# Performance work log

Hardware: AMD Instinct MI355X
Metric: run time of the kernel (lower is better)

The kernel has to match this reference:

```python
import jax, jax.numpy as jnp
import numpy as np

N, E, G = 50000, 500000, 64
IN, HID, HEADS, DH, OUT = 128, 128, 8, 16, 256


def setup_inputs() -> dict:
    key = jax.random.key(0)
    ks = jax.random.split(key, 20)
    w = lambda k, s, sc=0.05: jax.random.normal(k, s, dtype=jnp.float32) * sc
    return {
        'feature': jax.random.normal(ks[0], (N, IN), dtype=jnp.float32),
        'W_gc1': w(ks[1], (IN, HID)), 'b_gc1': jnp.zeros((HID,), jnp.float32),
        'W_gc2': w(ks[2], (HID, HID)), 'b_gc2': jnp.zeros((HID,), jnp.float32),
        'W_src': w(ks[3], (3, HID, HID)), 'b_src': jnp.zeros((3, HID), jnp.float32),
        'W_dst': w(ks[4], (3, HID, HID)), 'b_dst': jnp.zeros((3, HID), jnp.float32),
        'attn': w(ks[5], (3, HEADS, DH), 0.1),
        'Wc1': w(ks[6], (HID, HID)), 'bc1': jnp.zeros((HID,), jnp.float32),
        'Wc2': w(ks[7], (HID, HID // 2)), 'bc2': jnp.zeros((HID // 2,), jnp.float32),
        'Wc3': w(ks[8], (HID // 2, OUT)), 'bc3': jnp.zeros((OUT,), jnp.float32),
        'src': jax.random.randint(ks[9], (E,), 0, N, dtype=jnp.int32),
        'dst': jax.random.randint(ks[10], (E,), 0, N, dtype=jnp.int32),
        'node2graph': jnp.sort(jax.random.randint(ks[11], (N,), 0, G, dtype=jnp.int32)),
    }


def reference(feature, W_gc1, b_gc1, W_gc2, b_gc2, W_src, b_src, W_dst, b_dst, attn,
              Wc1, bc1, Wc2, bc2, Wc3, bc3, src, dst, node2graph):
    ones = jnp.ones((E,), jnp.float32)
    # DGL GraphConv norm='both': src normalized by out-degree, dst by in-degree
    ns = jnp.maximum(jax.ops.segment_sum(ones, src, N), 1.0) ** -0.5
    nd = jnp.maximum(jax.ops.segment_sum(ones, dst, N), 1.0) ** -0.5

    def graph_conv(h, W, b):
        m = (h * ns[:, None]) @ W                 # mult W before aggregation (in>=out)
        agg = jax.ops.segment_sum(m[src], dst, N) # copy_u + sum reduce
        return agg * nd[:, None] + b

    h = jax.nn.relu(graph_conv(feature, W_gc1, b_gc1))
    h = jax.nn.relu(graph_conv(h, W_gc2, b_gc2))

    def gatv2(h, Ws, bs, Wd, bd, a):
        fs = (h @ Ws + bs).reshape(N, HEADS, DH)
        fd = (h @ Wd + bd).reshape(N, HEADS, DH)
        e = jax.nn.leaky_relu(fs[src] + fd[dst], 0.2)   # [E,H,D]
        logit = jnp.einsum('ehd,hd->eh', e, a)          # [E,H]
        m = jax.ops.segment_max(logit, dst, N)          # edge-softmax over dst
        p = jnp.exp(logit - m[dst])
        s = jax.ops.segment_sum(p, dst, N)
        alpha = p / s[dst]                              # [E,H]
        out = jax.ops.segment_sum(alpha[:, :, None] * fs[src], dst, N)
        out = out + h.reshape(N, HEADS, DH)             # identity residual (in==H*D)
        return jax.nn.relu(out).reshape(N, HID)

    for i in range(3):
        h = gatv2(h, W_src[i], b_src[i], W_dst[i], b_dst[i], attn[i])

    hg = jax.ops.segment_max(h, node2graph, G)          # dgl.max_nodes -> [G,HID]
    z = jax.nn.relu(hg @ Wc1 + bc1)
    z = jax.nn.relu(z @ Wc2 + bc2)
    return z @ Wc3 + bc3
```

## Files before the change

kernel.cpp:

```cpp
#include <hip/hip_runtime.h>
#include <hip/hip_bf16.h>

#define NN 50000
#define EE 500000
#define GG 64
#define HIDD 128
#define HEADS 8
#define DHH 16
#define NBLK ((NN + 255) / 256)
#define RTILES 3128
#define GEMM_GRID 391

typedef __bf16 bf16x8 __attribute__((ext_vector_type(8)));
typedef float f32x4 __attribute__((ext_vector_type(4)));

__device__ inline float rowsum8(float y) {
  int t;
  t = __builtin_amdgcn_mov_dpp(__float_as_int(y), 0xB1, 0xF, 0xF, true);  y += __int_as_float(t);
  t = __builtin_amdgcn_mov_dpp(__float_as_int(y), 0x4E, 0xF, 0xF, true);  y += __int_as_float(t);
  t = __builtin_amdgcn_mov_dpp(__float_as_int(y), 0x141, 0xF, 0xF, true); y += __int_as_float(t);
  return y;
}

__device__ inline float2 unpk2(unsigned u) {
  return make_float2(__uint_as_float(u << 16), __uint_as_float(u & 0xFFFF0000u));
}

__device__ inline int frag_off(int row, int kc) {
  return (row >> 4) * 2048 + (kc >> 2) * 512 + ((row & 15) + (kc & 3) * 16) * 8;
}

__global__ void deg_kernel(const int* __restrict__ src, const int* __restrict__ dst,
                           int* __restrict__ outdeg, int* __restrict__ indeg) {
  int i = blockIdx.x * blockDim.x + threadIdx.x;
  int stride = gridDim.x * blockDim.x;
  for (; i < EE; i += stride) {
    atomicAdd(&outdeg[src[i]], 1);
    atomicAdd(&indeg[dst[i]], 1);
  }
}

__global__ void norm_kernel(const int* __restrict__ outdeg, float* __restrict__ ns) {
  int i = blockIdx.x * blockDim.x + threadIdx.x;
  if (i < NN) ns[i] = rsqrtf((float)max(outdeg[i], 1));
}

__global__ __launch_bounds__(256) void scan1_kernel(const int* __restrict__ deg,
                                                    int* __restrict__ excl,
                                                    int* __restrict__ bsum) {
  __shared__ int buf[256];
  int t = threadIdx.x;
  int idx = blockIdx.x * 256 + t;
  int v = (idx < NN) ? deg[idx] : 0;
  buf[t] = v;
  __syncthreads();
#pragma unroll
  for (int off = 1; off < 256; off <<= 1) {
    int tmp = (t >= off) ? buf[t - off] : 0;
    __syncthreads();
    buf[t] += tmp;
    __syncthreads();
  }
  if (idx < NN) excl[idx] = buf[t] - v;
  if (t == 255) bsum[blockIdx.x] = buf[255];
}

__global__ __launch_bounds__(256) void scan2_kernel(int* __restrict__ bsum) {
  __shared__ int buf[256];
  int t = threadIdx.x;
  int v = (t < NBLK) ? bsum[t] : 0;
  buf[t] = v;
  __syncthreads();
#pragma unroll
  for (int off = 1; off < 256; off <<= 1) {
    int tmp = (t >= off) ? buf[t - off] : 0;
    __syncthreads();
    buf[t] += tmp;
    __syncthreads();
  }
  if (t < NBLK) bsum[t] = buf[t] - v;
}

__global__ __launch_bounds__(256) void scan3_kernel(int* __restrict__ excl,
                                                    const int* __restrict__ bsum,
                                                    int* __restrict__ cursor) {
  int idx = blockIdx.x * 256 + threadIdx.x;
  if (idx < NN) {
    int v = excl[idx] + bsum[blockIdx.x];
    excl[idx] = v;
    cursor[idx] = v;
  }
}

__global__ void bin_kernel(const int* __restrict__ src, const int* __restrict__ dst,
                           int* __restrict__ cursor, int* __restrict__ csr_src) {
  int i = blockIdx.x * blockDim.x + threadIdx.x;
  int stride = gridDim.x * blockDim.x;
  for (; i < EE; i += stride) {
    int pos = atomicAdd(&cursor[dst[i]], 1);
    csr_src[pos] = src[i];
  }
}

__global__ __launch_bounds__(256) void split_w_kernel(
    const float* __restrict__ W_gc1, const float* __restrict__ W_gc2,
    const float* __restrict__ W_src, const float* __restrict__ W_dst,
    __bf16* __restrict__ Wblk)
{
  int tid = blockIdx.x * 256 + threadIdx.x;
  int m = tid >> 14;
  int kn = tid & 16383;
  int k = kn >> 7, n = kn & 127;
  const float* Wm = (m == 0) ? W_gc1 : (m == 1) ? W_gc2
                   : (m < 5) ? (W_src + (m - 2) * 16384) : (W_dst + (m - 5) * 16384);
  float v = Wm[kn];
  __bf16 h = (__bf16)v;
  __bf16 l = (__bf16)(v - (float)h);
  int ks = k >> 5;
  int L = n * 32 + ((k >> 3) & 3) * 8 + (k & 7);
  int swz = L ^ ((n & 7) << 3);
  __bf16* dstp = Wblk + m * 32768 + ks * 8192;
  dstp[swz] = h;
  dstp[4096 + swz] = l;
}

__global__ __launch_bounds__(256) void split_h_kernel(
    const float* __restrict__ X, const float* __restrict__ scale,
    __bf16* __restrict__ Ah, __bf16* __restrict__ Al)
{
  int tid = blockIdx.x * 256 + threadIdx.x;
  int row = tid >> 4, kc = tid & 15;
  float v[8];
  if (row < NN) {
    const float4* p = (const float4*)(X + row * 128 + kc * 8);
    float4 a = p[0], b = p[1];
    float s = scale ? scale[row] : 1.f;
    v[0] = a.x * s; v[1] = a.y * s; v[2] = a.z * s; v[3] = a.w * s;
    v[4] = b.x * s; v[5] = b.y * s; v[6] = b.z * s; v[7] = b.w * s;
  } else {
#pragma unroll
    for (int i = 0; i < 8; ++i) v[i] = 0.f;
  }
  bf16x8 hi, lo;
#pragma unroll
  for (int i = 0; i < 8; ++i) {
    __bf16 h = (__bf16)v[i];
    hi[i] = h;
    lo[i] = (__bf16)(v[i] - (float)h);
  }
  int off = frag_off(row, kc);
  *(bf16x8*)(Ah + off) = hi;
  *(bf16x8*)(Al + off) = lo;
}

__global__ __launch_bounds__(256) void gemm_mfma(
    const __bf16* __restrict__ Ah, const __bf16* __restrict__ Al,
    const __bf16* __restrict__ Wmat, const float* __restrict__ bias,
    __bf16* __restrict__ outb)
{
  __shared__ __bf16 wt[8192];
  int tid = threadIdx.x;
  int wid = tid >> 6, lane = tid & 63;
  int wr = wid >> 1, wc = wid & 1;
  int l15 = lane & 15, l4 = lane >> 4;
  f32x4 acc[4][4];
#pragma unroll
  for (int a = 0; a < 4; ++a)
#pragma unroll
    for (int b = 0; b < 4; ++b) acc[a][b] = (f32x4){0.f, 0.f, 0.f, 0.f};
  int rowtile0 = blockIdx.x * 8 + wr * 4;

  for (int ks = 0; ks < 4; ++ks) {
    {
      const bf16x8* g = (const bf16x8*)(Wmat + ks * 8192);
      bf16x8* l = (bf16x8*)wt;
      l[tid]       = g[tid];
      l[tid + 256] = g[tid + 256];
      l[tid + 512] = g[tid + 512];
      l[tid + 768] = g[tid + 768];
    }
    bf16x8 ah[4], al[4];
#pragma unroll
    for (int rt = 0; rt < 4; ++rt) {
      int off = (rowtile0 + rt) * 2048 + ks * 512 + lane * 8;
      ah[rt] = *(const bf16x8*)(Ah + off);
      al[rt] = *(const bf16x8*)(Al + off);
    }
    __syncthreads();
#pragma unroll
    for (int ct = 0; ct < 4; ++ct) {
      int n = wc * 64 + ct * 16 + l15;
      int ei = (n * 32 + l4 * 8) ^ ((n & 7) << 3);
      bf16x8 bh = *(const bf16x8*)(wt + ei);
      bf16x8 bl = *(const bf16x8*)(wt + 4096 + ei);
#pragma unroll
      for (int rt = 0; rt < 4; ++rt) {
        acc[rt][ct] = __builtin_amdgcn_mfma_f32_16x16x32_bf16(ah[rt], bh, acc[rt][ct], 0, 0, 0);
        acc[rt][ct] = __builtin_amdgcn_mfma_f32_16x16x32_bf16(ah[rt], bl, acc[rt][ct], 0, 0, 0);
        acc[rt][ct] = __builtin_amdgcn_mfma_f32_16x16x32_bf16(al[rt], bh, acc[rt][ct], 0, 0, 0);
      }
    }
    __syncthreads();
  }
  int rowbase = blockIdx.x * 128 + wr * 64;
#pragma unroll
  for (int ct = 0; ct < 4; ++ct) {
    int col = wc * 64 + ct * 16 + l15;
    float b = bias ? bias[col] : 0.f;
#pragma unroll
    for (int rt = 0; rt < 4; ++rt) {
#pragma unroll
      for (int r = 0; r < 4; ++r) {
        int row = rowbase + rt * 16 + l4 * 4 + r;
        if (row < NN) outb[row * 128 + col] = (__bf16)(acc[rt][ct][r] + b);
      }
    }
  }
}

__global__ __launch_bounds__(64) void gc_agg_kernel(
    const __bf16* __restrict__ mb, const int* __restrict__ rowoff,
    const int* __restrict__ indeg, const int* __restrict__ csr_src,
    const float2* __restrict__ bias2, const float* __restrict__ nsrow,
    float2* __restrict__ out2,
    __bf16* __restrict__ Ah, __bf16* __restrict__ Al)
{
  __shared__ float buf[128];
  int d = blockIdx.x, c = threadIdx.x;
  int ro = rowoff[d], dg = indeg[d];
  float2 a0 = {0.f, 0.f}, a1 = {0.f, 0.f}, a2 = {0.f, 0.f}, a3 = {0.f, 0.f};
  int j = 0;
  for (; j + 4 <= dg; j += 4) {
    int s0 = csr_src[ro + j], s1 = csr_src[ro + j + 1];
    int s2 = csr_src[ro + j + 2], s3 = csr_src[ro + j + 3];
    float2 v0 = unpk2(*(const unsigned*)(mb + s0 * 128 + 2 * c));
    float2 v1 = unpk2(*(const unsigned*)(mb + s1 * 128 + 2 * c));
    float2 v2 = unpk2(*(const unsigned*)(mb + s2 * 128 + 2 * c));
    float2 v3 = unpk2(*(const unsigned*)(mb + s3 * 128 + 2 * c));
    a0.x += v0.x; a0.y += v0.y; a1.x += v1.x; a1.y += v1.y;
    a2.x += v2.x; a2.y += v2.y; a3.x += v3.x; a3.y += v3.y;
  }
  for (; j < dg; ++j) {
    float2 v = unpk2(*(const unsigned*)(mb + csr_src[ro + j] * 128 + 2 * c));
    a0.x += v.x; a0.y += v.y;
  }
  float accx = (a0.x + a1.x) + (a2.x + a3.x);
  float accy = (a0.y + a1.y) + (a2.y + a3.y);
  float ndv = rsqrtf((float)max(dg, 1));
  float2 b = bias2[c];
  float vx = fmaxf(accx * ndv + b.x, 0.f);
  float vy = fmaxf(accy * ndv + b.y, 0.f);
  if (out2) out2[d * 64 + c] = make_float2(vx, vy);
  if (Ah) {
    float s = nsrow ? nsrow[d] : 1.f;
    ((float2*)buf)[c] = make_float2(vx * s, vy * s);
    __syncthreads();
    if (c < 32) {
      int kc = c & 15;
      int off = frag_off(d, kc);
      bf16x8 pk;
      if (c < 16) {
#pragma unroll
        for (int i = 0; i < 8; ++i) pk[i] = (__bf16)buf[kc * 8 + i];
        *(bf16x8*)(Ah + off) = pk;
      } else {
#pragma unroll
        for (int i = 0; i < 8; ++i) {
          float x = buf[kc * 8 + i];
          __bf16 hh = (__bf16)x;
          pk[i] = (__bf16)(x - (float)hh);
        }
        *(bf16x8*)(Al + off) = pk;
      }
    }
  }
}

__global__ __launch_bounds__(64) void gat_node_kernel(
    const __bf16* __restrict__ fsb,
    const __bf16* __restrict__ fdb,
    const float* __restrict__ attn,
    const int* __restrict__ rowoff, const int* __restrict__ indeg,
    const int* __restrict__ csr_src,
    float2* __restrict__ h2,
    __bf16* __restrict__ Ah, __bf16* __restrict__ Al)
{
  __shared__ float buf[128];
  int d = blockIdx.x, c = threadIdx.x;
  int ro = rowoff[d], dg = indeg[d];
  float2 fdp = unpk2(*(const unsigned*)(fdb + d * 128 + 2 * c));
  float2 ap = ((const float2*)attn)[c];
  float mA = -INFINITY, sA = 0.f; float2 aA = {0.f, 0.f};
  float mB = -INFINITY, sB = 0.f; float2 aB = {0.f, 0.f};
  int j = 0;
  for (; j + 2 <= dg; j += 2) {
    int s0 = csr_src[ro + j], s1 = csr_src[ro + j + 1];
    float2 f0 = unpk2(*(const unsigned*)(fsb + s0 * 128 + 2 * c));
    float2 f1 = unpk2(*(const unsigned*)(fsb + s1 * 128 + 2 * c));
    float x0 = f0.x + fdp.x; x0 = fmaxf(x0, 0.f) + 0.2f * fminf(x0, 0.f);
    float z0 = f0.y + fdp.y; z0 = fmaxf(z0, 0.f) + 0.2f * fminf(z0, 0.f);
    float x1 = f1.x + fdp.x; x1 = fmaxf(x1, 0.f) + 0.2f * fminf(x1, 0.f);
    float z1 = f1.y + fdp.y; z1 = fmaxf(z1, 0.f) + 0.2f * fminf(z1, 0.f);
    float y0 = rowsum8(ap.x * x0 + ap.y * z0);
    float y1 = rowsum8(ap.x * x1 + ap.y * z1);
    float nm = fmaxf(mA, y0);
    float sc = __expf(mA - nm), p = __expf(y0 - nm);
    sA = sA * sc + p; aA.x = aA.x * sc + p * f0.x; aA.y = aA.y * sc + p * f0.y; mA = nm;
    nm = fmaxf(mB, y1);
    sc = __expf(mB - nm); p = __expf(y1 - nm);
    sB = sB * sc + p; aB.x = aB.x * sc + p * f1.x; aB.y = aB.y * sc + p * f1.y; mB = nm;
  }
  if (j < dg) {
    int s0 = csr_src[ro + j];
    float2 f0 = unpk2(*(const unsigned*)(fsb + s0 * 128 + 2 * c));
    float x0 = f0.x + fdp.x; x0 = fmaxf(x0, 0.f) + 0.2f * fminf(x0, 0.f);
    float z0 = f0.y + fdp.y; z0 = fmaxf(z0, 0.f) + 0.2f * fminf(z0, 0.f);
    float y0 = rowsum8(ap.x * x0 + ap.y * z0);
    float nm = fmaxf(mA, y0);
    float sc = __expf(mA - nm), p = __expf(y0 - nm);
    sA = sA * sc + p; aA.x = aA.x * sc + p * f0.x; aA.y = aA.y * sc + p * f0.y; mA = nm;
  }
  float ox = 0.f, oy = 0.f;
  if (dg > 0) {
    float M = fmaxf(mA, mB);
    float eA = __expf(mA - M), eB = __expf(mB - M);
    float inv = 1.f / (sA * eA + sB * eB);
    ox = (aA.x * eA + aB.x * eB) * inv;
    oy = (aA.y * eA + aB.y * eB) * inv;
  }
  float2 hv = h2[d * 64 + c];
  float vx = fmaxf(ox + hv.x, 0.f);
  float vy = fmaxf(oy + hv.y, 0.f);
  h2[d * 64 + c] = make_float2(vx, vy);
  if (Ah) {
    ((float2*)buf)[c] = make_float2(vx, vy);
    __syncthreads();
    if (c < 32) {
      int kc = c & 15;
      int off = frag_off(d, kc);
      bf16x8 pk;
      if (c < 16) {
#pragma unroll
        for (int i = 0; i < 8; ++i) pk[i] = (__bf16)buf[kc * 8 + i];
        *(bf16x8*)(Ah + off) = pk;
      } else {
#pragma unroll
        for (int i = 0; i < 8; ++i) {
          float x = buf[kc * 8 + i];
          __bf16 hh = (__bf16)x;
          pk[i] = (__bf16)(x - (float)hh);
        }
        *(bf16x8*)(Al + off) = pk;
      }
    }
  }
}

__global__ __launch_bounds__(128) void pool_kernel(const float* __restrict__ h,
                                                   const int* __restrict__ n2g,
                                                   unsigned* __restrict__ hg)
{
  int g = blockIdx.x >> 3, chunk = blockIdx.x & 7, c = threadIdx.x;
  int lo = 0, hi = NN;
  while (lo < hi) { int mid = (lo + hi) >> 1; if (n2g[mid] < g) lo = mid + 1; else hi = mid; }
  int start = lo;
  hi = NN;
  while (lo < hi) { int mid = (lo + hi) >> 1; if (n2g[mid] < g + 1) lo = mid + 1; else hi = mid; }
  int end = lo;
  int len = end - start;
  int s = start + (int)(((long long)len * chunk) >> 3);
  int e = start + (int)(((long long)len * (chunk + 1)) >> 3);
  float m = 0.f;
  for (int r = s; r < e; ++r) m = fmaxf(m, h[r * 128 + c]);
  atomicMax(&hg[g * 128 + c], __float_as_uint(m));
}

__global__ __launch_bounds__(128) void mlp_kernel(
    const float* __restrict__ hg,
    const float* __restrict__ Wc1, const float* __restrict__ bc1,
    const float* __restrict__ Wc2, const float* __restrict__ bc2,
    const float* __restrict__ Wc3, const float* __restrict__ bc3,
    float* __restrict__ out)
{
  __shared__ float x[128], z1[128], z2[64];
  int g = blockIdx.x, t = threadIdx.x;
  x[t] = hg[g * 128 + t];
  __syncthreads();
  float acc = bc1[t];
  for (int k = 0; k < 128; ++k) acc += x[k] * Wc1[k * 128 + t];
  z1[t] = fmaxf(acc, 0.f);
  __syncthreads();
  if (t < 64) {
    float a2 = bc2[t];
    for (int k = 0; k < 128; ++k) a2 += z1[k] * Wc2[k * 64 + t];
    z2[t] = fmaxf(a2, 0.f);
  }
  __syncthreads();
#pragma unroll
  for (int p = 0; p < 2; ++p) {
    int c = t + p * 128;
    float a3 = bc3[c];
    for (int k = 0; k < 64; ++k) a3 += z2[k] * Wc3[k * 256 + c];
    out[g * 256 + c] = a3;
  }
}

extern "C" void kernel_launch(void* const* d_in, const int* in_sizes, int n_in,
                              void* d_out, int out_size, void* d_ws, size_t ws_size,
                              hipStream_t stream)
{
  const float* feature = (const float*)d_in[0];
  const float* W_gc1 = (const float*)d_in[1];
  const float* b_gc1 = (const float*)d_in[2];
  const float* W_gc2 = (const float*)d_in[3];
  const float* b_gc2 = (const float*)d_in[4];
  const float* W_src = (const float*)d_in[5];
  const float* b_src = (const float*)d_in[6];
  const float* W_dst = (const float*)d_in[7];
  const float* b_dst = (const float*)d_in[8];
  const float* attn  = (const float*)d_in[9];
  const float* Wc1 = (const float*)d_in[10];
  const float* bc1 = (const float*)d_in[11];
  const float* Wc2 = (const float*)d_in[12];
  const float* bc2 = (const float*)d_in[13];
  const float* Wc3 = (const float*)d_in[14];
  const float* bc3 = (const float*)d_in[15];
  const int* src = (const int*)d_in[16];
  const int* dst = (const int*)d_in[17];
  const int* n2g = (const int*)d_in[18];

  char* base = (char*)d_ws;
  int* indeg  = (int*)base;            base += NN * sizeof(int);
  int* outdeg = (int*)base;            base += NN * sizeof(int);
  int* rowoff = (int*)base;            base += NN * sizeof(int);
  int* cursor = (int*)base;            base += NN * sizeof(int);
  int* bsum   = (int*)base;            base += 256 * sizeof(int);
  int* csr_src = (int*)base;           base += EE * sizeof(int);
  float* ns = (float*)base;            base += NN * sizeof(float);
  float* h0 = (float*)base;            base += (size_t)NN * HIDD * sizeof(float);
  __bf16* fsb = (__bf16*)base;         base += (size_t)NN * HIDD * sizeof(__bf16);
  __bf16* fdb = (__bf16*)base;         base += (size_t)NN * HIDD * sizeof(__bf16);
  __bf16* mb  = (__bf16*)base;         base += (size_t)NN * HIDD * sizeof(__bf16);
  __bf16* Ah = (__bf16*)base;          base += (size_t)RTILES * 2048 * sizeof(__bf16);
  __bf16* Al = (__bf16*)base;          base += (size_t)RTILES * 2048 * sizeof(__bf16);
  __bf16* Wblk = (__bf16*)base;        base += (size_t)8 * 32768 * sizeof(__bf16);
  float* hg = (float*)base;            base += GG * HIDD * sizeof(float);

  hipMemsetAsync(indeg, 0, 2 * NN * sizeof(int), stream);
  deg_kernel<<<2048, 256, 0, stream>>>(src, dst, outdeg, indeg);
  norm_kernel<<<NBLK, 256, 0, stream>>>(outdeg, ns);
  scan1_kernel<<<NBLK, 256, 0, stream>>>(indeg, rowoff, bsum);
  scan2_kernel<<<1, 256, 0, stream>>>(bsum);
  scan3_kernel<<<NBLK, 256, 0, stream>>>(rowoff, bsum, cursor);
  bin_kernel<<<2048, 256, 0, stream>>>(src, dst, cursor, csr_src);

  split_w_kernel<<<512, 256, 0, stream>>>(W_gc1, W_gc2, W_src, W_dst, Wblk);

  const int split_grid = RTILES * 16 * 16 / 256;

  split_h_kernel<<<split_grid, 256, 0, stream>>>(feature, ns, Ah, Al);
  gemm_mfma<<<GEMM_GRID, 256, 0, stream>>>(Ah, Al, Wblk + 0 * 32768, nullptr, mb);
  gc_agg_kernel<<<NN, 64, 0, stream>>>(mb, rowoff, indeg, csr_src,
                                       (const float2*)b_gc1, ns, nullptr, Ah, Al);
  gemm_mfma<<<GEMM_GRID, 256, 0, stream>>>(Ah, Al, Wblk + 1 * 32768, nullptr, mb);
  gc_agg_kernel<<<NN, 64, 0, stream>>>(mb, rowoff, indeg, csr_src,
                                       (const float2*)b_gc2, nullptr, (float2*)h0, Ah, Al);

  for (int i = 0; i < 3; ++i) {
    gemm_mfma<<<GEMM_GRID, 256, 0, stream>>>(Ah, Al, Wblk + (2 + i) * 32768, b_src + i * HIDD, fsb);
    gemm_mfma<<<GEMM_GRID, 256, 0, stream>>>(Ah, Al, Wblk + (5 + i) * 32768, b_dst + i * HIDD, fdb);
    bool last = (i == 2);
    gat_node_kernel<<<NN, 64, 0, stream>>>(fsb, fdb,
                                           attn + i * HEADS * DHH,
                                           rowoff, indeg, csr_src, (float2*)h0,
                                           last ? nullptr : Ah, last ? nullptr : Al);
  }

  hipMemsetAsync(hg, 0, GG * HIDD * sizeof(float), stream);
  pool_kernel<<<GG * 8, 128, 0, stream>>>(h0, n2g, (unsigned*)hg);
  mlp_kernel<<<GG, 128, 0, stream>>>(hg, Wc1, bc1, Wc2, bc2, Wc3, bc3, (float*)d_out);
}
```

Baseline: 505.2 us.

## Fuse src/dst GAT GEMMs, unroll attention loop, read residual from split bf16

```diff
diff --git a/kernel.cpp b/kernel.cpp
--- a/kernel.cpp
+++ b/kernel.cpp
@@ -153,12 +153,11 @@
   *(bf16x8*)(Al + off) = lo;
 }
 
-__global__ __launch_bounds__(256) void gemm_mfma(
+__device__ inline void gemm_body(
     const __bf16* __restrict__ Ah, const __bf16* __restrict__ Al,
     const __bf16* __restrict__ Wmat, const float* __restrict__ bias,
-    __bf16* __restrict__ outb)
-{
-  __shared__ __bf16 wt[8192];
+    __bf16* __restrict__ outb, int bx, __bf16* wt)
+{
   int tid = threadIdx.x;
   int wid = tid >> 6, lane = tid & 63;
   int wr = wid >> 1, wc = wid & 1;
@@ -168,7 +167,7 @@
   for (int a = 0; a < 4; ++a)
 #pragma unroll
     for (int b = 0; b < 4; ++b) acc[a][b] = (f32x4){0.f, 0.f, 0.f, 0.f};
-  int rowtile0 = blockIdx.x * 8 + wr * 4;
+  int rowtile0 = bx * 8 + wr * 4;
 
   for (int ks = 0; ks < 4; ++ks) {
     {
@@ -202,7 +201,7 @@
     }
     __syncthreads();
   }
-  int rowbase = blockIdx.x * 128 + wr * 64;
+  int rowbase = bx * 128 + wr * 64;
 #pragma unroll
   for (int ct = 0; ct < 4; ++ct) {
     int col = wc * 64 + ct * 16 + l15;
@@ -218,11 +217,32 @@
   }
 }
 
+__global__ __launch_bounds__(256) void gemm_mfma(
+    const __bf16* __restrict__ Ah, const __bf16* __restrict__ Al,
+    const __bf16* __restrict__ Wmat, const float* __restrict__ bias,
+    __bf16* __restrict__ outb)
+{
+  __shared__ __bf16 wt[8192];
+  gemm_body(Ah, Al, Wmat, bias, outb, blockIdx.x, wt);
+}
+
+__global__ __launch_bounds__(256) void gemm_dual(
+    const __bf16* __restrict__ Ah, const __bf16* __restrict__ Al,
+    const __bf16* __restrict__ W0, const __bf16* __restrict__ W1,
+    const float* __restrict__ bias0, const float* __restrict__ bias1,
+    __bf16* __restrict__ out0, __bf16* __restrict__ out1)
+{
+  __shared__ __bf16 wt[8192];
+  int which = (blockIdx.x >= GEMM_GRID);
+  int bx = blockIdx.x - (which ? GEMM_GRID : 0);
+  gemm_body(Ah, Al, which ? W1 : W0, which ? bias1 : bias0,
+            which ? out1 : out0, bx, wt);
+}
+
 __global__ __launch_bounds__(64) void gc_agg_kernel(
     const __bf16* __restrict__ mb, const int* __restrict__ rowoff,
     const int* __restrict__ indeg, const int* __restrict__ csr_src,
     const float2* __restrict__ bias2, const float* __restrict__ nsrow,
-    float2* __restrict__ out2,
     __bf16* __restrict__ Ah, __bf16* __restrict__ Al)
 {
   __shared__ float buf[128];
@@ -250,28 +270,25 @@
   float2 b = bias2[c];
   float vx = fmaxf(accx * ndv + b.x, 0.f);
   float vy = fmaxf(accy * ndv + b.y, 0.f);
-  if (out2) out2[d * 64 + c] = make_float2(vx, vy);
-  if (Ah) {
-    float s = nsrow ? nsrow[d] : 1.f;
-    ((float2*)buf)[c] = make_float2(vx * s, vy * s);
-    __syncthreads();
-    if (c < 32) {
-      int kc = c & 15;
-      int off = frag_off(d, kc);
-      bf16x8 pk;
-      if (c < 16) {
-#pragma unroll
-        for (int i = 0; i < 8; ++i) pk[i] = (__bf16)buf[kc * 8 + i];
-        *(bf16x8*)(Ah + off) = pk;
-      } else {
-#pragma unroll
-        for (int i = 0; i < 8; ++i) {
-          float x = buf[kc * 8 + i];
-          __bf16 hh = (__bf16)x;
-          pk[i] = (__bf16)(x - (float)hh);
-        }
-        *(bf16x8*)(Al + off) = pk;
+  float s = nsrow ? nsrow[d] : 1.f;
+  ((float2*)buf)[c] = make_float2(vx * s, vy * s);
+  __syncthreads();
+  if (c < 32) {
+    int kc = c & 15;
+    int off = frag_off(d, kc);
+    bf16x8 pk;
+    if (c < 16) {
+#pragma unroll
+      for (int i = 0; i < 8; ++i) pk[i] = (__bf16)buf[kc * 8 + i];
+      *(bf16x8*)(Ah + off) = pk;
+    } else {
+#pragma unroll
+      for (int i = 0; i < 8; ++i) {
+        float x = buf[kc * 8 + i];
+        __bf16 hh = (__bf16)x;
+        pk[i] = (__bf16)(x - (float)hh);
       }
+      *(bf16x8*)(Al + off) = pk;
     }
   }
 }
@@ -282,8 +299,8 @@
     const float* __restrict__ attn,
     const int* __restrict__ rowoff, const int* __restrict__ indeg,
     const int* __restrict__ csr_src,
-    float2* __restrict__ h2,
-    __bf16* __restrict__ Ah, __bf16* __restrict__ Al)
+    __bf16* __restrict__ Ah, __bf16* __restrict__ Al,
+    float2* __restrict__ out2)
 {
   __shared__ float buf[128];
   int d = blockIdx.x, c = threadIdx.x;
@@ -292,25 +309,39 @@
   float2 ap = ((const float2*)attn)[c];
   float mA = -INFINITY, sA = 0.f; float2 aA = {0.f, 0.f};
   float mB = -INFINITY, sB = 0.f; float2 aB = {0.f, 0.f};
+  float mC = -INFINITY, sC = 0.f; float2 aC = {0.f, 0.f};
+  float mD = -INFINITY, sD = 0.f; float2 aD = {0.f, 0.f};
   int j = 0;
-  for (; j + 2 <= dg; j += 2) {
-    int s0 = csr_src[ro + j], s1 = csr_src[ro + j + 1];
+  for (; j + 4 <= dg; j += 4) {
+    int s0 = csr_src[ro + j],     s1 = csr_src[ro + j + 1];
+    int s2 = csr_src[ro + j + 2], s3 = csr_src[ro + j + 3];
     float2 f0 = unpk2(*(const unsigned*)(fsb + s0 * 128 + 2 * c));
     float2 f1 = unpk2(*(const unsigned*)(fsb + s1 * 128 + 2 * c));
+    float2 f2 = unpk2(*(const unsigned*)(fsb + s2 * 128 + 2 * c));
+    float2 f3 = unpk2(*(const unsigned*)(fsb + s3 * 128 + 2 * c));
     float x0 = f0.x + fdp.x; x0 = fmaxf(x0, 0.f) + 0.2f * fminf(x0, 0.f);
     float z0 = f0.y + fdp.y; z0 = fmaxf(z0, 0.f) + 0.2f * fminf(z0, 0.f);
     float x1 = f1.x + fdp.x; x1 = fmaxf(x1, 0.f) + 0.2f * fminf(x1, 0.f);
     float z1 = f1.y + fdp.y; z1 = fmaxf(z1, 0.f) + 0.2f * fminf(z1, 0.f);
+    float x2 = f2.x + fdp.x; x2 = fmaxf(x2, 0.f) + 0.2f * fminf(x2, 0.f);
+    float z2 = f2.y + fdp.y; z2 = fmaxf(z2, 0.f) + 0.2f * fminf(z2, 0.f);
+    float x3 = f3.x + fdp.x; x3 = fmaxf(x3, 0.f) + 0.2f * fminf(x3, 0.f);
+    float z3 = f3.y + fdp.y; z3 = fmaxf(z3, 0.f) + 0.2f * fminf(z3, 0.f);
     float y0 = rowsum8(ap.x * x0 + ap.y * z0);
     float y1 = rowsum8(ap.x * x1 + ap.y * z1);
-    float nm = fmaxf(mA, y0);
-    float sc = __expf(mA - nm), p = __expf(y0 - nm);
+    float y2 = rowsum8(ap.x * x2 + ap.y * z2);
+    float y3 = rowsum8(ap.x * x3 + ap.y * z3);
+    float nm, sc, p;
+    nm = fmaxf(mA, y0); sc = __expf(mA - nm); p = __expf(y0 - nm);
     sA = sA * sc + p; aA.x = aA.x * sc + p * f0.x; aA.y = aA.y * sc + p * f0.y; mA = nm;
-    nm = fmaxf(mB, y1);
-    sc = __expf(mB - nm); p = __expf(y1 - nm);
+    nm = fmaxf(mB, y1); sc = __expf(mB - nm); p = __expf(y1 - nm);
     sB = sB * sc + p; aB.x = aB.x * sc + p * f1.x; aB.y = aB.y * sc + p * f1.y; mB = nm;
-  }
-  if (j < dg) {
+    nm = fmaxf(mC, y2); sc = __expf(mC - nm); p = __expf(y2 - nm);
+    sC = sC * sc + p; aC.x = aC.x * sc + p * f2.x; aC.y = aC.y * sc + p * f2.y; mC = nm;
+    nm = fmaxf(mD, y3); sc = __expf(mD - nm); p = __expf(y3 - nm);
+    sD = sD * sc + p; aD.x = aD.x * sc + p * f3.x; aD.y = aD.y * sc + p * f3.y; mD = nm;
+  }
+  for (; j < dg; ++j) {
     int s0 = csr_src[ro + j];
     float2 f0 = unpk2(*(const unsigned*)(fsb + s0 * 128 + 2 * c));
     float x0 = f0.x + fdp.x; x0 = fmaxf(x0, 0.f) + 0.2f * fminf(x0, 0.f);
@@ -320,19 +351,23 @@
     float sc = __expf(mA - nm), p = __expf(y0 - nm);
     sA = sA * sc + p; aA.x = aA.x * sc + p * f0.x; aA.y = aA.y * sc + p * f0.y; mA = nm;
   }
+  int rbase = frag_off(d, c >> 2) + ((2 * c) & 7);
+  float2 rh = unpk2(*(const unsigned*)(Ah + rbase));
+  float2 rl = unpk2(*(const unsigned*)(Al + rbase));
   float ox = 0.f, oy = 0.f;
   if (dg > 0) {
-    float M = fmaxf(mA, mB);
+    float M = fmaxf(fmaxf(mA, mB), fmaxf(mC, mD));
     float eA = __expf(mA - M), eB = __expf(mB - M);
-    float inv = 1.f / (sA * eA + sB * eB);
-    ox = (aA.x * eA + aB.x * eB) * inv;
-    oy = (aA.y * eA + aB.y * eB) * inv;
-  }
-  float2 hv = h2[d * 64 + c];
-  float vx = fmaxf(ox + hv.x, 0.f);
-  float vy = fmaxf(oy + hv.y, 0.f);
-  h2[d * 64 + c] = make_float2(vx, vy);
-  if (Ah) {
+    float eC = __expf(mC - M), eD = __expf(mD - M);
+    float inv = 1.f / (sA * eA + sB * eB + sC * eC + sD * eD);
+    ox = (aA.x * eA + aB.x * eB + aC.x * eC + aD.x * eD) * inv;
+    oy = (aA.y * eA + aB.y * eB + aC.y * eC + aD.y * eD) * inv;
+  }
+  float vx = fmaxf(ox + (rh.x + rl.x), 0.f);
+  float vy = fmaxf(oy + (rh.y + rl.y), 0.f);
+  if (out2) {
+    out2[d * 64 + c] = make_float2(vx, vy);
+  } else {
     ((float2*)buf)[c] = make_float2(vx, vy);
     __syncthreads();
     if (c < 32) {
@@ -461,19 +496,20 @@
   split_h_kernel<<<split_grid, 256, 0, stream>>>(feature, ns, Ah, Al);
   gemm_mfma<<<GEMM_GRID, 256, 0, stream>>>(Ah, Al, Wblk + 0 * 32768, nullptr, mb);
   gc_agg_kernel<<<NN, 64, 0, stream>>>(mb, rowoff, indeg, csr_src,
-                                       (const float2*)b_gc1, ns, nullptr, Ah, Al);
+                                       (const float2*)b_gc1, ns, Ah, Al);
   gemm_mfma<<<GEMM_GRID, 256, 0, stream>>>(Ah, Al, Wblk + 1 * 32768, nullptr, mb);
   gc_agg_kernel<<<NN, 64, 0, stream>>>(mb, rowoff, indeg, csr_src,
-                                       (const float2*)b_gc2, nullptr, (float2*)h0, Ah, Al);
+                                       (const float2*)b_gc2, nullptr, Ah, Al);
 
   for (int i = 0; i < 3; ++i) {
-    gemm_mfma<<<GEMM_GRID, 256, 0, stream>>>(Ah, Al, Wblk + (2 + i) * 32768, b_src + i * HIDD, fsb);
-    gemm_mfma<<<GEMM_GRID, 256, 0, stream>>>(Ah, Al, Wblk + (5 + i) * 32768, b_dst + i * HIDD, fdb);
+    gemm_dual<<<2 * GEMM_GRID, 256, 0, stream>>>(Ah, Al,
+        Wblk + (2 + i) * 32768, Wblk + (5 + i) * 32768,
+        b_src + i * HIDD, b_dst + i * HIDD, fsb, fdb);
     bool last = (i == 2);
     gat_node_kernel<<<NN, 64, 0, stream>>>(fsb, fdb,
                                            attn + i * HEADS * DHH,
-                                           rowoff, indeg, csr_src, (float2*)h0,
-                                           last ? nullptr : Ah, last ? nullptr : Al);
+                                           rowoff, indeg, csr_src, Ah, Al,
+                                           last ? (float2*)h0 : nullptr);
   }
 
   hipMemsetAsync(hg, 0, GG * HIDD * sizeof(float), stream);
```

After: 710.9 us. 1.41x slower.
